# Kernel tuning notes

Hardware: AMD Instinct MI355X
Metric: run time of the kernel (lower is better)

The kernel has to match this reference:

```python
import jax, jax.numpy as jnp
import numpy as np

DEGREE = 2
STEPS = 7
N_FEATURES = 120
R_TARGETS = 4
LATENT = 4
D = N_FEATURES + R_TARGETS + LATENT          # 128: padded state dim
N_POLY = 1 + D + D * D                       # 16513: sum_{k=0..degree} D^k for degree=2
BATCH = 16384
W_SCALE = 1e-4                               # keep the iterated quadratic map stable


def setup_inputs() -> dict:
    key = jax.random.key(0)
    k1, k2 = jax.random.split(key)
    X = jax.random.normal(k1, (BATCH, N_FEATURES), dtype=jnp.float32)
    W = jax.random.normal(k2, (N_POLY, D), dtype=jnp.float32) * W_SCALE
    t_init = jnp.zeros((R_TARGETS,), dtype=jnp.float32)
    l_init = jnp.zeros((LATENT,), dtype=jnp.float32)
    return {"X": X, "W": W, "t_init": t_init, "l_init": l_init}


def _poly_full(x):
    """PolynomialFeatures via repeated outer products: [1, x, vec(x xp_{k-1}^T), ...]."""
    n = x.shape[0]
    xp = [jnp.ones((n, 1), x.dtype), x]
    for _ in range(2, DEGREE + 1):
        # [n, D, 1] * [n, 1, P] -> [n, D*P]  (matches tf: X @ expand_dims(XP[-1],1))
        xp.append((x[:, :, None] * xp[-1][:, None, :]).reshape(n, -1))
    return jnp.concatenate(xp, axis=-1)  # [n, N_POLY]


def reference(X, W, t_init, l_init):
    # pad inputs with r_targets + latent_units zeros, then add init values
    inits = jnp.concatenate([jnp.zeros((N_FEATURES,), X.dtype), t_init, l_init])
    x0 = jnp.pad(X, ((0, 0), (0, R_TARGETS + LATENT))) + inits  # [B, D]

    def step(x, _):
        return x + _poly_full(x) @ W, None  # TaylorMap: residual + poly GEMM

    x, _ = jax.lax.scan(step, x0, None, length=STEPS)
    # self._targets = target_features + appended extra target dims
    return x[:, N_FEATURES:N_FEATURES + R_TARGETS]  # [B, n_targets]
```

## Files before the change

kernel.cpp:

```cpp
#include <hip/hip_runtime.h>
#include <hip/hip_bf16.h>


#define DSTATE 128
#define BATCH  16384
#define NSTEPS 7
#define BT     64
#define NSL    585

typedef __attribute__((ext_vector_type(8)))  short  short8;
typedef __attribute__((ext_vector_type(16))) float  f32x16;

__device__ __forceinline__ unsigned short f2bf(float f){
    unsigned int u = __float_as_uint(f);
    u += 0x7fff + ((u >> 16) & 1);
    return (unsigned short)(u >> 16);
}

__global__ void prep_kernel(const float* __restrict__ W, short8* __restrict__ A){
    int gid = blockIdx.x * 256 + threadIdx.x;
    const int ntotal = 4 * 130 * 8 * 64;
    if (gid >= ntotal) return;
    int lane = gid & 63; int r = gid >> 6;
    int s = r & 7;  r >>= 3;
    int row = r % 130;
    int t   = r / 130;
    int d  = t * 32 + (lane & 31);
    int kb = (lane >> 5) * 8;
    int dst;
    bool zero = false;
    if (row < 64){
        int sl = row >> 4;
        if (s < sl) return;
        dst = t * NSL + 9 * row + (s - sl);
    } else if (row < 128){
        int p  = 127 - row;
        int sl = row >> 4;
        if (s < sl) return;
        int ca = 8 - (p >> 4);
        dst = t * NSL + 9 * p + ca + (s - sl);
    } else if (row == 128){
        dst = t * NSL + 576 + s;
    } else {
        if (s) return;
        dst = t * NSL + 584;
        zero = true;
    }
    union { short8 v; unsigned short u[8]; } fr;
#pragma unroll
    for (int e = 0; e < 8; ++e){
        int j = s * 16 + kb + e;
        float v;
        if (zero) v = 0.0f;
        else if (row < 128){
            if      (j < row)  v = 0.0f;
            else if (j == row) v = W[(129 + 128 * row + j) * 128 + d];
            else               v = W[(129 + 128 * row + j) * 128 + d]
                                 + W[(129 + 128 * j + row) * 128 + d];
        } else {
            v = W[(1 + j) * 128 + d];
        }
        fr.u[e] = f2bf(v);
    }
    A[(size_t)dst * 64 + lane] = fr.v;
}

__global__ __launch_bounds__(512)
void taylor_kernel(const float* __restrict__ X, const float* __restrict__ W,
                   const float* __restrict__ tini, const float* __restrict__ lini,
                   const short8* __restrict__ A, float* __restrict__ out)
{
    __shared__ float  x_lds[DSTATE * BT];
    __shared__ float  w0_lds[DSTATE];
    __shared__ short8 bpack[2 * 8 * 64];
    __shared__ float  sc_lds[2][4 * 64 * 17];

    const int tid  = threadIdx.x;
    const int lane = tid & 63;
    const int w    = tid >> 6;
    const int t    = w & 3;
    const int g    = w >> 2;
    const int ln   = lane & 31;
    const int hi   = lane >> 5;
    const int b0   = blockIdx.x * BT;

#pragma unroll
    for (int it = 0; it < 16; ++it){
        int entry = tid + it * 512;
        int b = entry >> 7, d = entry & 127;
        float v;
        if      (d < 120) v = X[(b0 + b) * 120 + d];
        else if (d < 124) v = tini[d - 120];
        else              v = lini[d - 124];
        x_lds[d * BT + b] = v;
    }
    if (tid < DSTATE) w0_lds[tid] = W[tid];

    const short8* const Aw = A + ((size_t)t * NSL + (size_t)g * 288) * 64 + lane;
    const f32x16 zero16 = {};

#pragma unroll 1
    for (int step = 0; step < NSTEPS; ++step){
        __syncthreads();

        const bool active = (step < NSTEPS - 1) || (t == 3);

        const short8* ap = Aw;
        short8 abuf[9];
        if (active){
#pragma unroll
            for (int s = 0; s < 9; ++s) abuf[s] = ap[s * 64];
            ap += 9 * 64;
        }

#pragma unroll
        for (int f0 = 0; f0 < 2; ++f0){
            int f  = tid + f0 * 512;
            int gg = f >> 9, s = (f >> 6) & 7, l = f & 63;
            int c  = gg * 32 + (l & 31);
            int jb = 16 * s + 8 * (l >> 5);
            union { short8 v; unsigned short u[8]; } fr;
#pragma unroll
            for (int e = 0; e < 8; ++e)
                fr.u[e] = f2bf(x_lds[(jb + e) * BT + c]);
            bpack[f] = fr.v;
        }

        f32x16 acc0, acc1;
        if (active){
            if (g == 0){
#pragma unroll
                for (int r = 0; r < 16; ++r){
                    int d = 32 * t + (r & 3) + 8 * (r >> 2) + 4 * hi;
                    acc0[r] = x_lds[d * BT + ln]      + w0_lds[d];
                    acc1[r] = x_lds[d * BT + 32 + ln] + w0_lds[d];
                }
            } else {
#pragma unroll
                for (int r = 0; r < 16; ++r){ acc0[r] = 0.f; acc1[r] = 0.f; }
            }
        }

        __syncthreads();

        if (active){
            short8 bfrag0[8], bfrag1[8];

#define PAIRS(BK)                                                               \
            {                                                                   \
                _Pragma("unroll")                                               \
                for (int s = 0; s < 8 - (BK); ++s){                             \
                    bfrag0[s] = bpack[((BK) + s) * 64 + lane];                  \
                    bfrag1[s] = bpack[512 + ((BK) + s) * 64 + lane];            \
                }                                                               \
                _Pragma("unroll 2")                                             \
                for (int q = 0; q < 16; ++q){                                   \
                    const int p = 16 * (BK) + q;                                \
                    float s0a = x_lds[p * BT + ln];                             \
                    float s0b = x_lds[p * BT + 32 + ln];                        \
                    float s1a = x_lds[(127 - p) * BT + ln];                     \
                    float s1b = x_lds[(127 - p) * BT + 32 + ln];                \
                    f32x16 Y0, Y1;                                              \
                    _Pragma("unroll")                                           \
                    for (int s = 0; s < 8 - (BK); ++s){                         \
                        Y0 = __builtin_amdgcn_mfma_f32_32x32x16_bf16(abuf[s], bfrag0[s], s ? Y0 : zero16, 0, 0, 0); \
                        Y1 = __builtin_amdgcn_mfma_f32_32x32x16_bf16(abuf[s], bfrag1[s], s ? Y1 : zero16, 0, 0, 0); \
                        abuf[s] = ap[s * 64];                                   \
                    }                                                           \
                    acc0 += s0a * Y0;                                           \
                    acc1 += s0b * Y1;                                           \
                    f32x16 Z0, Z1;                                              \
                    _Pragma("unroll")                                           \
                    for (int s = 0; s < 1 + (BK); ++s){                         \
                        Z0 = __builtin_amdgcn_mfma_f32_32x32x16_bf16(abuf[8 - (BK) + s], bfrag0[7 - 2 * (BK) + s], s ? Z0 : zero16, 0, 0, 0); \
                        Z1 = __builtin_amdgcn_mfma_f32_32x32x16_bf16(abuf[8 - (BK) + s], bfrag1[7 - 2 * (BK) + s], s ? Z1 : zero16, 0, 0, 0); \
                        abuf[8 - (BK) + s] = ap[(8 - (BK) + s) * 64];           \
                    }                                                           \
                    acc0 += s1a * Z0;                                           \
                    acc1 += s1b * Z1;                                           \
                    ap += 9 * 64;                                               \
                }                                                               \
            }

            if (g == 0){
                PAIRS(0) PAIRS(1)
            } else {
                PAIRS(2) PAIRS(3)
#pragma unroll
                for (int s = 0; s < 8; ++s){
                    bfrag0[s] = bpack[s * 64 + lane];
                    bfrag1[s] = bpack[512 + s * 64 + lane];
                }
#pragma unroll
                for (int s = 0; s < 8; ++s){
                    acc0 = __builtin_amdgcn_mfma_f32_32x32x16_bf16(abuf[s], bfrag0[s], acc0, 0, 0, 0);
                    acc1 = __builtin_amdgcn_mfma_f32_32x32x16_bf16(abuf[s], bfrag1[s], acc1, 0, 0, 0);
                }
#pragma unroll
                for (int r = 0; r < 16; ++r){
                    sc_lds[0][(t * 64 + lane) * 17 + r] = acc0[r];
                    sc_lds[1][(t * 64 + lane) * 17 + r] = acc1[r];
                }
            }
#undef PAIRS
        }

        __syncthreads();
        if (active && g == 0){
#pragma unroll
            for (int r = 0; r < 16; ++r){
                acc0[r] += sc_lds[0][(t * 64 + lane) * 17 + r];
                acc1[r] += sc_lds[1][(t * 64 + lane) * 17 + r];
            }
            if (step < NSTEPS - 1){
#pragma unroll
                for (int r = 0; r < 16; ++r){
                    int d = 32 * t + (r & 3) + 8 * (r >> 2) + 4 * hi;
                    x_lds[d * BT + ln]      = acc0[r];
                    x_lds[d * BT + 32 + ln] = acc1[r];
                }
            } else if (hi == 0){
                *(float4*)(out + (size_t)(b0 + ln) * 4) =
                    make_float4(acc0[12], acc0[13], acc0[14], acc0[15]);
                *(float4*)(out + (size_t)(b0 + 32 + ln) * 4) =
                    make_float4(acc1[12], acc1[13], acc1[14], acc1[15]);
            }
        }
    }
}

extern "C" void kernel_launch(void* const* d_in, const int* in_sizes, int n_in,
                              void* d_out, int out_size, void* d_ws, size_t ws_size,
                              hipStream_t stream)
{
    const float* X  = (const float*)d_in[0];
    const float* W  = (const float*)d_in[1];
    const float* ti = (const float*)d_in[2];
    const float* li = (const float*)d_in[3];
    float* out      = (float*)d_out;
    short8* A       = (short8*)d_ws;

    const int ntotal = 4 * 130 * 8 * 64;
    prep_kernel<<<(ntotal + 255) / 256, 256, 0, stream>>>(W, A);
    taylor_kernel<<<BATCH / BT, 512, 0, stream>>>(X, W, ti, li, A, out);
}
```

Baseline: 311.3 us.

## Stream packed weights through LDS ring with global_load_lds shared across batch halves

Changes the work split from K-halves (with a cross-group LDS reduction) to batch-column halves. Each wave group now owns 32 batch columns and walks the full K range. The packed bf16 weight fragments are now brought in through a triple-buffered LDS ring filled by global_load_lds, with both groups cooperatively loading the slices they share. This is meant to halve global/L2 weight traffic per block and remove the partial-sum exchange. In exchange it adds a block barrier per pair iteration (65 per step), which may stall the MFMA pipeline.

```diff
diff --git a/kernel.cpp b/kernel.cpp
--- a/kernel.cpp
+++ b/kernel.cpp
@@ -16,6 +16,15 @@
     u += 0x7fff + ((u >> 16) & 1);
     return (unsigned short)(u >> 16);
 }
+
+__device__ __forceinline__ void barrier_lgkm(){
+    asm volatile("s_waitcnt lgkmcnt(0)" ::: "memory");
+    __builtin_amdgcn_s_barrier();
+}
+
+#define GLL(gp, lp) __builtin_amdgcn_global_load_lds(                           \
+        (const __attribute__((address_space(1))) void*)(gp),                    \
+        (__attribute__((address_space(3))) void*)(lp), 16, 0, 0)
 
 __global__ void prep_kernel(const float* __restrict__ W, short8* __restrict__ A){
     int gid = blockIdx.x * 256 + threadIdx.x;
@@ -73,16 +82,39 @@
     __shared__ float  x_lds[DSTATE * BT];
     __shared__ float  w0_lds[DSTATE];
     __shared__ short8 bpack[2 * 8 * 64];
-    __shared__ float  sc_lds[2][4 * 64 * 17];
+    __shared__ short8 ring[3][4][9][64];
 
     const int tid  = threadIdx.x;
     const int lane = tid & 63;
     const int w    = tid >> 6;
     const int t    = w & 3;
-    const int g    = w >> 2;
+    const int ch   = w >> 2;
     const int ln   = lane & 31;
     const int hi   = lane >> 5;
     const int b0   = blockIdx.x * BT;
+    const int c0   = 32 * ch;
+
+    const char* const Atl = (const char*)A + ((size_t)t * NSL * 64 + lane) * 16;
+
+#define ISSUE(SRCP, SL)                                                         \
+    {                                                                           \
+        const char* gb_ = Atl + (size_t)(9 * (SRCP)) * 1024;                    \
+        if (ch == 0){                                                           \
+            _Pragma("unroll")                                                   \
+            for (int s2 = 0; s2 < 5; ++s2)                                      \
+                GLL(gb_ + s2 * 1024, &ring[SL][t][s2][0]);                      \
+        } else {                                                                \
+            _Pragma("unroll")                                                   \
+            for (int s2 = 5; s2 < 9; ++s2)                                      \
+                GLL(gb_ + s2 * 1024, &ring[SL][t][s2][0]);                      \
+        }                                                                       \
+    }
+#define WAITV()                                                                 \
+    { if (ch == 0) asm volatile("s_waitcnt vmcnt(5)" ::: "memory");             \
+      else         asm volatile("s_waitcnt vmcnt(4)" ::: "memory"); }
+
+    ISSUE(0, 0)
+    ISSUE(1, 1)
 
 #pragma unroll
     for (int it = 0; it < 16; ++it){
@@ -96,21 +128,23 @@
     }
     if (tid < DSTATE) w0_lds[tid] = W[tid];
 
-    const short8* const Aw = A + ((size_t)t * NSL + (size_t)g * 288) * 64 + lane;
+    WAITV();
+
     const f32x16 zero16 = {};
+    short8 abuf[9];
+    short8 bfrag[8];
+    f32x16 acc;
+    int o1 = 1;
 
 #pragma unroll 1
     for (int step = 0; step < NSTEPS; ++step){
-        __syncthreads();
+        barrier_lgkm();
 
         const bool active = (step < NSTEPS - 1) || (t == 3);
 
-        const short8* ap = Aw;
-        short8 abuf[9];
-        if (active){
-#pragma unroll
-            for (int s = 0; s < 9; ++s) abuf[s] = ap[s * 64];
-            ap += 9 * 64;
+        if (step == 0){
+#pragma unroll
+            for (int s = 0; s < 9; ++s) abuf[s] = ring[0][t][s][lane];
         }
 
 #pragma unroll
@@ -126,107 +160,90 @@
             bpack[f] = fr.v;
         }
 
-        f32x16 acc0, acc1;
         if (active){
-            if (g == 0){
+#pragma unroll
+            for (int r = 0; r < 16; ++r){
+                int d = 32 * t + (r & 3) + 8 * (r >> 2) + 4 * hi;
+                acc[r] = x_lds[d * BT + c0 + ln] + w0_lds[d];
+            }
+        }
+
+        barrier_lgkm();
+
+        if (active){
+#pragma unroll
+            for (int s = 0; s < 8; ++s)
+                bfrag[s] = bpack[ch * 512 + s * 64 + lane];
+        }
+
+#define PBLOCK(BK)                                                              \
+        _Pragma("unroll 2")                                                     \
+        for (int q = 0; q < 16; ++q){                                           \
+            const int p = 16 * (BK) + q;                                        \
+            int o2 = (o1 == 2) ? 0 : o1 + 1;                                    \
+            if (active){                                                        \
+                int srcp = (p == 63) ? 0 : p + 2;      \
+                ISSUE(srcp, o2)                                                 \
+                WAITV()                                                         \
+            }                                                                   \
+            barrier_lgkm();                       \
+            if (active){                                                        \
+                float s0 = x_lds[p * BT + c0 + ln];                             \
+                float s1 = x_lds[(127 - p) * BT + c0 + ln];                     \
+                f32x16 Y;                                                       \
+                _Pragma("unroll")                                               \
+                for (int s = 0; s < 8 - (BK); ++s){                             \
+                    Y = __builtin_amdgcn_mfma_f32_32x32x16_bf16(abuf[s], bfrag[(BK) + s], s ? Y : zero16, 0, 0, 0); \
+                    abuf[s] = ring[o1][t][s][lane];                             \
+                }                                                               \
+                acc += s0 * Y;                                                  \
+                f32x16 Z;                                                       \
+                _Pragma("unroll")                                               \
+                for (int s = 0; s < 1 + (BK); ++s){                             \
+                    Z = __builtin_amdgcn_mfma_f32_32x32x16_bf16(abuf[8 - (BK) + s], bfrag[7 - (BK) + s], s ? Z : zero16, 0, 0, 0); \
+                    abuf[8 - (BK) + s] = ring[o1][t][8 - (BK) + s][lane];       \
+                }                                                               \
+                acc += s1 * Z;                                                  \
+            }                                                                   \
+            o1 = o2;                                                            \
+        }
+
+        PBLOCK(0) PBLOCK(1) PBLOCK(2) PBLOCK(3)
+#undef PBLOCK
+
+        {
+            int o2 = (o1 == 2) ? 0 : o1 + 1;
+            if (active){
+                ISSUE(1, o2)
+                WAITV()
+            }
+            barrier_lgkm();
+            if (active){
+#pragma unroll
+                for (int s = 0; s < 8; ++s){
+                    acc = __builtin_amdgcn_mfma_f32_32x32x16_bf16(abuf[s], bfrag[s], acc, 0, 0, 0);
+                    abuf[s] = ring[o1][t][s][lane];
+                }
+                abuf[8] = ring[o1][t][8][lane];
+            }
+            o1 = o2;
+        }
+
+        if (active){
+            if (step < NSTEPS - 1){
 #pragma unroll
                 for (int r = 0; r < 16; ++r){
                     int d = 32 * t + (r & 3) + 8 * (r >> 2) + 4 * hi;
-                    acc0[r] = x_lds[d * BT + ln]      + w0_lds[d];
-                    acc1[r] = x_lds[d * BT + 32 + ln] + w0_lds[d];
-                }
-            } else {
-#pragma unroll
-                for (int r = 0; r < 16; ++r){ acc0[r] = 0.f; acc1[r] = 0.f; }
-            }
-        }
-
-        __syncthreads();
-
-        if (active){
-            short8 bfrag0[8], bfrag1[8];
-
-#define PAIRS(BK)                                                               \
-            {                                                                   \
-                _Pragma("unroll")                                               \
-                for (int s = 0; s < 8 - (BK); ++s){                             \
-                    bfrag0[s] = bpack[((BK) + s) * 64 + lane];                  \
-                    bfrag1[s] = bpack[512 + ((BK) + s) * 64 + lane];            \
-                }                                                               \
-                _Pragma("unroll 2")                                             \
-                for (int q = 0; q < 16; ++q){                                   \
-                    const int p = 16 * (BK) + q;                                \
-                    float s0a = x_lds[p * BT + ln];                             \
-                    float s0b = x_lds[p * BT + 32 + ln];                        \
-                    float s1a = x_lds[(127 - p) * BT + ln];                     \
-                    float s1b = x_lds[(127 - p) * BT + 32 + ln];                \
-                    f32x16 Y0, Y1;                                              \
-                    _Pragma("unroll")                                           \
-                    for (int s = 0; s < 8 - (BK); ++s){                         \
-                        Y0 = __builtin_amdgcn_mfma_f32_32x32x16_bf16(abuf[s], bfrag0[s], s ? Y0 : zero16, 0, 0, 0); \
-                        Y1 = __builtin_amdgcn_mfma_f32_32x32x16_bf16(abuf[s], bfrag1[s], s ? Y1 : zero16, 0, 0, 0); \
-                        abuf[s] = ap[s * 64];                                   \
-                    }                                                           \
-                    acc0 += s0a * Y0;                                           \
-                    acc1 += s0b * Y1;                                           \
-                    f32x16 Z0, Z1;                                              \
-                    _Pragma("unroll")                                           \
-                    for (int s = 0; s < 1 + (BK); ++s){                         \
-                        Z0 = __builtin_amdgcn_mfma_f32_32x32x16_bf16(abuf[8 - (BK) + s], bfrag0[7 - 2 * (BK) + s], s ? Z0 : zero16, 0, 0, 0); \
-                        Z1 = __builtin_amdgcn_mfma_f32_32x32x16_bf16(abuf[8 - (BK) + s], bfrag1[7 - 2 * (BK) + s], s ? Z1 : zero16, 0, 0, 0); \
-                        abuf[8 - (BK) + s] = ap[(8 - (BK) + s) * 64];           \
-                    }                                                           \
-                    acc0 += s1a * Z0;                                           \
-                    acc1 += s1b * Z1;                                           \
-                    ap += 9 * 64;                                               \
-                }                                                               \
-            }
-
-            if (g == 0){
-                PAIRS(0) PAIRS(1)
-            } else {
-                PAIRS(2) PAIRS(3)
-#pragma unroll
-                for (int s = 0; s < 8; ++s){
-                    bfrag0[s] = bpack[s * 64 + lane];
-                    bfrag1[s] = bpack[512 + s * 64 + lane];
-                }
-#pragma unroll
-                for (int s = 0; s < 8; ++s){
-                    acc0 = __builtin_amdgcn_mfma_f32_32x32x16_bf16(abuf[s], bfrag0[s], acc0, 0, 0, 0);
-                    acc1 = __builtin_amdgcn_mfma_f32_32x32x16_bf16(abuf[s], bfrag1[s], acc1, 0, 0, 0);
-                }
-#pragma unroll
-                for (int r = 0; r < 16; ++r){
-                    sc_lds[0][(t * 64 + lane) * 17 + r] = acc0[r];
-                    sc_lds[1][(t * 64 + lane) * 17 + r] = acc1[r];
-                }
-            }
-#undef PAIRS
-        }
-
-        __syncthreads();
-        if (active && g == 0){
-#pragma unroll
-            for (int r = 0; r < 16; ++r){
-                acc0[r] += sc_lds[0][(t * 64 + lane) * 17 + r];
-                acc1[r] += sc_lds[1][(t * 64 + lane) * 17 + r];
-            }
-            if (step < NSTEPS - 1){
-#pragma unroll
-                for (int r = 0; r < 16; ++r){
-                    int d = 32 * t + (r & 3) + 8 * (r >> 2) + 4 * hi;
-                    x_lds[d * BT + ln]      = acc0[r];
-                    x_lds[d * BT + 32 + ln] = acc1[r];
+                    x_lds[d * BT + c0 + ln] = acc[r];
                 }
             } else if (hi == 0){
-                *(float4*)(out + (size_t)(b0 + ln) * 4) =
-                    make_float4(acc0[12], acc0[13], acc0[14], acc0[15]);
-                *(float4*)(out + (size_t)(b0 + 32 + ln) * 4) =
-                    make_float4(acc1[12], acc1[13], acc1[14], acc1[15]);
-            }
-        }
-    }
+                *(float4*)(out + (size_t)(b0 + c0 + ln) * 4) =
+                    make_float4(acc[12], acc[13], acc[14], acc[15]);
+            }
+        }
+    }
+#undef ISSUE
+#undef WAITV
 }
 
 extern "C" void kernel_launch(void* const* d_in, const int* in_sizes, int n_in,
```

Result: slower. 371.9 us (+19.5%).
